# Performance work log

Hardware: AMD Instinct MI355X
Metric: run time of the kernel (lower is better)

The kernel has to match this reference:

```python
import jax, jax.numpy as jnp
import numpy as np

I_SIZE = 512
H_SIZE = 1024


def _wn(v, g):
    # weight_norm: W = g * v / ||v|| per output row (dim=0 in torch => norm over input dim)
    return v * (g / jnp.linalg.norm(v, axis=1))[:, None]


def setup_inputs() -> dict:
    key = jax.random.key(0)
    ks = jax.random.split(key, 8)
    B, S, I, H = 16, 512, I_SIZE, H_SIZE
    s_i = 1.0 / np.sqrt(I)
    s_h = 1.0 / np.sqrt(H)
    return {
        "x": jax.random.normal(ks[0], (B, S, I), jnp.float32),
        "mask": jnp.ones((B, S), jnp.float32),
        "wmx_v": jax.random.uniform(ks[1], (H, I), jnp.float32, -s_i, s_i),
        "wmx_g": jnp.ones((H,), jnp.float32),
        "wmh_v": jax.random.uniform(ks[2], (H, H), jnp.float32, -s_h, s_h),
        "wmh_g": jnp.ones((H,), jnp.float32),
        "wx_v": jax.random.uniform(ks[3], (4 * H, I), jnp.float32, -s_i, s_i),
        "wx_g": jnp.ones((4 * H,), jnp.float32),
        "wh_v": jax.random.uniform(ks[4], (4 * H, H), jnp.float32, -s_h, s_h),
        "wh_g": jnp.ones((4 * H,), jnp.float32),
        "wh_b": jax.random.uniform(ks[5], (4 * H,), jnp.float32, -s_h, s_h),
    }


def reference(x, mask, wmx_v, wmx_g, wmh_v, wmh_g, wx_v, wx_g, wh_v, wh_g, wh_b):
    B, S, _ = x.shape
    H = wmh_v.shape[0]
    Wmx = _wn(wmx_v, wmx_g)  # [H, I]
    Wmh = _wn(wmh_v, wmh_g)  # [H, H]
    Wx = _wn(wx_v, wx_g)     # [4H, I]
    Wh = _wn(wh_v, wh_g)     # [4H, H]

    # Precompute input-side projections in parallel over the whole sequence
    mx = jnp.einsum('bsi,hi->bsh', x, Wmx)   # [B, S, H]
    zx = jnp.einsum('bsi,pi->bsp', x, Wx)    # [B, S, 4H]
    mk = mask[:, :, None]                    # [B, S, 1]

    def step(carry, inp):
        h, c = carry
        mx_t, zx_t, m_t = inp
        m = mx_t * (h @ Wmh.T)
        z = zx_t + m @ Wh.T + wh_b
        i_, f_, o_, u_ = jnp.split(z, 4, axis=1)
        i_ = jax.nn.sigmoid(i_)
        f_ = jax.nn.sigmoid(f_)
        o_ = jax.nn.sigmoid(o_)
        u_ = jnp.tanh(u_)
        c_new = f_ * c + i_ * u_
        h_new = o_ * jnp.tanh(c_new)
        # masked blend: keep previous state where mask == 0
        h_new = m_t * h_new + (1.0 - m_t) * h
        c_new = m_t * c_new + (1.0 - m_t) * c
        return (h_new, c_new), h_new

    h0 = jnp.zeros((B, H), x.dtype)
    c0 = jnp.zeros((B, H), x.dtype)
    xs = (jnp.swapaxes(mx, 0, 1), jnp.swapaxes(zx, 0, 1), jnp.swapaxes(mk, 0, 1))
    (h_fin, c_fin), hs = jax.lax.scan(step, (h0, c0), xs)
    return jnp.swapaxes(hs, 0, 1), (h_fin, c_fin)
```

## Files before the change

kernel.cpp:

```cpp
#include <hip/hip_runtime.h>


typedef __attribute__((ext_vector_type(8))) short   short8;
typedef __attribute__((ext_vector_type(4))) float   float4_;

#define HSZ (16 * 512 * 1024)

__device__ __forceinline__ short f2bf(float x) {
  unsigned u = __float_as_uint(x);
  u += 0x7FFFu + ((u >> 16) & 1u);
  return (short)(u >> 16);
}
__device__ __forceinline__ float bf2f(unsigned short s) {
  return __uint_as_float(((unsigned)s) << 16);
}
__device__ __forceinline__ float sigf(float x) { return 1.f / (1.f + __expf(-x)); }
__device__ __forceinline__ float tanhfast(float x) { return 2.f / (1.f + __expf(-2.f * x)) - 1.f; }

__device__ __forceinline__ float4_ mfma16(short8 a, short8 b, float4_ c) {
  return __builtin_amdgcn_mfma_f32_16x16x32_bf16(a, b, c, 0, 0, 0);
}

__device__ __forceinline__ unsigned ld_flag(const unsigned* p) {
  return __hip_atomic_load(p, __ATOMIC_RELAXED, __HIP_MEMORY_SCOPE_AGENT);
}
__device__ __forceinline__ void st_agent(unsigned* p, unsigned v) {
  __hip_atomic_store(p, v, __ATOMIC_RELAXED, __HIP_MEMORY_SCOPE_AGENT);
}

__global__ __launch_bounds__(256) void wnorm_kernel(
    const float* __restrict__ v, const float* __restrict__ g,
    short* __restrict__ outH, short* __restrict__ outL, int cols, int permute)
{
  int r = blockIdx.x, tid = threadIdx.x;
  int src = r;
  if (permute) {
    int bid = r >> 4, jj = (r >> 2) & 3, gg = r & 3;
    src = gg * 1024 + bid * 4 + jj;
  }
  const float* row = v + (size_t)src * cols;
  float s = 0.f;
  for (int c = tid; c < cols; c += 256) { float x = row[c]; s += x * x; }
  #pragma unroll
  for (int off = 32; off; off >>= 1) s += __shfl_down(s, off);
  __shared__ float red[4];
  if ((tid & 63) == 0) red[tid >> 6] = s;
  __syncthreads();
  float tot = red[0] + red[1] + red[2] + red[3];
  float scale = g[src] / sqrtf(tot);
  for (int c = tid; c < cols; c += 256) {
    float wv = row[c] * scale;
    short hh = f2bf(wv);
    outH[(size_t)r * cols + c] = hh;
    outL[(size_t)r * cols + c] = f2bf(wv - bf2f((unsigned short)hh));
  }
}

template <int NCOLS>
__global__ __launch_bounds__(256) void gemm_xw(
    const float* __restrict__ X,
    const short* __restrict__ WH, const short* __restrict__ WL,
    float* __restrict__ Out)
{
  constexpr int BM = 128, BN = 64, BK = 32;
  __shared__ short Ah[BM][BK + 8], Al[BM][BK + 8];
  __shared__ short Bh[BN][BK + 8], Bl[BN][BK + 8];
  const int nT = NCOLS / BN;
  const int bm = blockIdx.x / nT, bn = blockIdx.x % nT;
  const int m0 = bm * BM, n0 = bn * BN;
  const int tid = threadIdx.x, lane = tid & 63, w = tid >> 6;
  const int lo = lane & 15, hi4 = lane >> 4;
  float4_ acc[2][4] = {};

  for (int kb = 0; kb < 512; kb += BK) {
    {
      int r = tid >> 1, kh = (tid & 1) << 4;
      const float* src = X + ((size_t)(m0 + r) << 9) + kb + kh;
      short8 h0, l0, h1, l1;
      #pragma unroll
      for (int u = 0; u < 8; ++u) {
        float xv = src[u];
        short hh = f2bf(xv);
        h0[u] = hh; l0[u] = f2bf(xv - bf2f((unsigned short)hh));
      }
      #pragma unroll
      for (int u = 0; u < 8; ++u) {
        float xv = src[8 + u];
        short hh = f2bf(xv);
        h1[u] = hh; l1[u] = f2bf(xv - bf2f((unsigned short)hh));
      }
      *(short8*)&Ah[r][kh] = h0;  *(short8*)&Ah[r][kh + 8] = h1;
      *(short8*)&Al[r][kh] = l0;  *(short8*)&Al[r][kh + 8] = l1;
    }
    {
      int cc = tid & 63, kq = tid >> 6;
      *(short8*)&Bh[cc][kq * 8] =
          *(const short8*)(WH + (size_t)(n0 + cc) * 512 + kb + kq * 8);
      *(short8*)&Bl[cc][kq * 8] =
          *(const short8*)(WL + (size_t)(n0 + cc) * 512 + kb + kq * 8);
    }
    __syncthreads();
    short8 bh[4], bl[4], ah[2], al[2];
    #pragma unroll
    for (int sn = 0; sn < 4; ++sn) {
      bh[sn] = *(const short8*)&Bh[sn * 16 + lo][hi4 * 8];
      bl[sn] = *(const short8*)&Bl[sn * 16 + lo][hi4 * 8];
    }
    #pragma unroll
    for (int sm = 0; sm < 2; ++sm) {
      ah[sm] = *(const short8*)&Ah[w * 32 + sm * 16 + lo][hi4 * 8];
      al[sm] = *(const short8*)&Al[w * 32 + sm * 16 + lo][hi4 * 8];
    }
    #pragma unroll
    for (int sm = 0; sm < 2; ++sm)
      #pragma unroll
      for (int sn = 0; sn < 4; ++sn)
        acc[sm][sn] = mfma16(ah[sm], bh[sn], acc[sm][sn]);
    #pragma unroll
    for (int sm = 0; sm < 2; ++sm)
      #pragma unroll
      for (int sn = 0; sn < 4; ++sn)
        acc[sm][sn] = mfma16(al[sm], bh[sn], acc[sm][sn]);
    #pragma unroll
    for (int sm = 0; sm < 2; ++sm)
      #pragma unroll
      for (int sn = 0; sn < 4; ++sn)
        acc[sm][sn] = mfma16(ah[sm], bl[sn], acc[sm][sn]);
    __syncthreads();
  }
  #pragma unroll
  for (int sm = 0; sm < 2; ++sm)
    #pragma unroll
    for (int sn = 0; sn < 4; ++sn)
      #pragma unroll
      for (int i = 0; i < 4; ++i) {
        int row = m0 + w * 32 + sm * 16 + hi4 * 4 + i;
        int col = n0 + sn * 16 + lo;
        Out[(size_t)row * NCOLS + col] = acc[sm][sn][i];
      }
}

__global__ __launch_bounds__(256, 1) void scan_kernel(
    const float* __restrict__ mx,
    const float* __restrict__ zx,
    const float* __restrict__ mask,
    const short* __restrict__ WmhH, const short* __restrict__ WmhL,
    const short* __restrict__ WhH,  const short* __restrict__ WhL,
    const float* __restrict__ bias,
    short* __restrict__ hbH, short* __restrict__ hbL,
    short* __restrict__ mbH, short* __restrict__ mbL,
    float* __restrict__ out,
    unsigned* __restrict__ flagA,
    unsigned* __restrict__ flagB)
{
  const int blk = blockIdx.x;
  const int tid = threadIdx.x;
  const int w = tid >> 6, lane = tid & 63;
  const int lo = lane & 15, hi4 = lane >> 4;

  if (blk < 16) {
    const int bid = blk * 4 + w;
    short8 wAh[32], wAl[32];
    {
      const short* wrH = WmhH + (size_t)(bid * 16 + lo) * 1024 + hi4 * 8;
      const short* wrL = WmhL + (size_t)(bid * 16 + lo) * 1024 + hi4 * 8;
      #pragma unroll
      for (int kc = 0; kc < 32; ++kc) {
        wAh[kc] = *(const short8*)(wrH + kc * 32);
        wAl[kc] = *(const short8*)(wrL + kc * 32);
      }
    }
    for (int t = 0; t < 512; ++t) {
      const int pp = t & 1, pq = pp ^ 1;
      float mxv[4];
      #pragma unroll
      for (int i = 0; i < 4; ++i)
        mxv[i] = mx[((size_t)((hi4 * 4 + i) * 512 + t)) * 1024 + bid * 16 + lo];

      if (w == 0) {
        const unsigned tgt = (unsigned)t;
        for (;;) {
          unsigned v = ld_flag(flagB + lane * 16);
          if (__all((int)(v >= tgt))) break;
          __builtin_amdgcn_s_sleep(1);
        }
      }
      __syncthreads();
      __builtin_amdgcn_fence(__ATOMIC_ACQUIRE, "agent");

      const short* hrH = hbH + pq * 16384 + lo * 1024 + hi4 * 8;
      const short* hrL = hbL + pq * 16384 + lo * 1024 + hi4 * 8;
      float4_ a0 = {0,0,0,0}, a1 = {0,0,0,0}, a2 = {0,0,0,0};
      float4_ a3 = {0,0,0,0}, a4 = {0,0,0,0}, a5 = {0,0,0,0};
      #pragma unroll
      for (int kc = 0; kc < 32; kc += 2) {
        short8 fh0 = *(const short8*)(hrH + (kc + 0) * 32);
        short8 fl0 = *(const short8*)(hrL + (kc + 0) * 32);
        short8 fh1 = *(const short8*)(hrH + (kc + 1) * 32);
        short8 fl1 = *(const short8*)(hrL + (kc + 1) * 32);
        a0 = mfma16(fh0, wAh[kc + 0], a0);
        a1 = mfma16(fl0, wAh[kc + 0], a1);
        a2 = mfma16(fh0, wAl[kc + 0], a2);
        a3 = mfma16(fh1, wAh[kc + 1], a3);
        a4 = mfma16(fl1, wAh[kc + 1], a4);
        a5 = mfma16(fh1, wAl[kc + 1], a5);
      }
      float4_ mres = ((a0 + a1) + (a2 + a3)) + (a4 + a5);
      #pragma unroll
      for (int i = 0; i < 4; ++i) {
        const int b = hi4 * 4 + i;
        float mv = mres[i] * mxv[i];
        short mh = f2bf(mv);
        short ml = f2bf(mv - bf2f((unsigned short)mh));
        unsigned hv = (unsigned short)mh, lv2 = (unsigned short)ml;
        unsigned hp = hv  | (((unsigned)__shfl_xor((int)hv, 1)) << 16);
        unsigned lp = lv2 | (((unsigned)__shfl_xor((int)lv2, 1)) << 16);
        if ((lo & 1) == 0) {
          st_agent((unsigned*)(mbH + pp * 16384 + b * 1024 + bid * 16 + lo), hp);
          st_agent((unsigned*)(mbL + pp * 16384 + b * 1024 + bid * 16 + lo), lp);
        }
      }
      asm volatile("s_waitcnt vmcnt(0)" ::: "memory");
      __syncthreads();
      if (tid == 0) st_agent(flagA + blk * 16, (unsigned)(t + 1));
    }
  } else {
    const int ebid = (blk - 16) * 4 + w;
    const int eb = lane >> 2, ejj = lane & 3;
    const int ej = ebid * 4 + ejj;
    float h_st = 0.f, c_st = 0.f;
    float biasr[4];
    #pragma unroll
    for (int g = 0; g < 4; ++g) biasr[g] = bias[g * 1024 + ebid * 4 + ejj];

    short8 wBh[32], wBl[32];
    {
      const int g = lo & 3, jj = lo >> 2;
      const short* wrH = WhH + (size_t)(g * 1024 + ebid * 4 + jj) * 1024 + hi4 * 8;
      const short* wrL = WhL + (size_t)(g * 1024 + ebid * 4 + jj) * 1024 + hi4 * 8;
      #pragma unroll
      for (int kc = 0; kc < 32; ++kc) {
        wBh[kc] = *(const short8*)(wrH + kc * 32);
        wBl[kc] = *(const short8*)(wrL + kc * 32);
      }
    }
    __shared__ float z_s[4][16][17];

    for (int t = 0; t < 512; ++t) {
      const int pp = t & 1;
      float4_ zv = *(const float4_*)(zx + (size_t)(eb * 512 + t) * 4096 + ebid * 16 + ejj * 4);
      float mk = mask[eb * 512 + t];

      if (w == 0) {
        const unsigned tgt = (unsigned)(t + 1);
        for (;;) {
          unsigned v = 0xFFFFFFFFu;
          if (lane < 16) v = ld_flag(flagA + lane * 16);
          if (__all((int)(v >= tgt))) break;
          __builtin_amdgcn_s_sleep(1);
        }
      }
      __syncthreads();
      __builtin_amdgcn_fence(__ATOMIC_ACQUIRE, "agent");

      const short* mrH = mbH + pp * 16384 + lo * 1024 + hi4 * 8;
      const short* mrL = mbL + pp * 16384 + lo * 1024 + hi4 * 8;
      float4_ b0 = {0,0,0,0}, b1 = {0,0,0,0}, b2 = {0,0,0,0};
      float4_ b3 = {0,0,0,0}, b4 = {0,0,0,0}, b5 = {0,0,0,0};
      #pragma unroll
      for (int kc = 0; kc < 32; kc += 2) {
        short8 fh0 = *(const short8*)(mrH + (kc + 0) * 32);
        short8 fl0 = *(const short8*)(mrL + (kc + 0) * 32);
        short8 fh1 = *(const short8*)(mrH + (kc + 1) * 32);
        short8 fl1 = *(const short8*)(mrL + (kc + 1) * 32);
        b0 = mfma16(fh0, wBh[kc + 0], b0);
        b1 = mfma16(fl0, wBh[kc + 0], b1);
        b2 = mfma16(fh0, wBl[kc + 0], b2);
        b3 = mfma16(fh1, wBh[kc + 1], b3);
        b4 = mfma16(fl1, wBh[kc + 1], b4);
        b5 = mfma16(fh1, wBl[kc + 1], b5);
      }
      float4_ zres = ((b0 + b1) + (b2 + b3)) + (b4 + b5);
      #pragma unroll
      for (int i = 0; i < 4; ++i) z_s[w][hi4 * 4 + i][lo] = zres[i];
      asm volatile("s_waitcnt lgkmcnt(0)" ::: "memory");

      float zg[4];
      #pragma unroll
      for (int g = 0; g < 4; ++g)
        zg[g] = z_s[w][eb][ejj * 4 + g] + zv[g] + biasr[g];
      float ig = sigf(zg[0]), fg = sigf(zg[1]), og = sigf(zg[2]);
      float ug = tanhfast(zg[3]);
      float cn = fg * c_st + ig * ug;
      float hn = og * tanhfast(cn);
      hn = mk * hn + (1.f - mk) * h_st;
      cn = mk * cn + (1.f - mk) * c_st;
      h_st = hn; c_st = cn;

      out[(size_t)(eb * 512 + t) * 1024 + ej] = hn;
      short hh = f2bf(hn);
      short hl = f2bf(hn - bf2f((unsigned short)hh));
      unsigned hv = (unsigned short)hh, lv2 = (unsigned short)hl;
      unsigned hp = hv  | (((unsigned)__shfl_xor((int)hv, 1)) << 16);
      unsigned lp = lv2 | (((unsigned)__shfl_xor((int)lv2, 1)) << 16);
      if ((ejj & 1) == 0) {
        st_agent((unsigned*)(hbH + pp * 16384 + eb * 1024 + ej), hp);
        st_agent((unsigned*)(hbL + pp * 16384 + eb * 1024 + ej), lp);
      }
      asm volatile("s_waitcnt vmcnt(0)" ::: "memory");
      __syncthreads();
      if (tid == 0) st_agent(flagB + (blk - 16) * 16, (unsigned)(t + 1));
    }
    out[HSZ + eb * 1024 + ej] = h_st;
    out[HSZ + 16384 + eb * 1024 + ej] = c_st;
  }
}

extern "C" void kernel_launch(void* const* d_in, const int* in_sizes, int n_in,
                              void* d_out, int out_size, void* d_ws, size_t ws_size,
                              hipStream_t stream)
{
  (void)in_sizes; (void)n_in; (void)out_size; (void)ws_size;
  const float* x     = (const float*)d_in[0];
  const float* mask  = (const float*)d_in[1];
  const float* wmx_v = (const float*)d_in[2];
  const float* wmx_g = (const float*)d_in[3];
  const float* wmh_v = (const float*)d_in[4];
  const float* wmh_g = (const float*)d_in[5];
  const float* wx_v  = (const float*)d_in[6];
  const float* wx_g  = (const float*)d_in[7];
  const float* wh_v  = (const float*)d_in[8];
  const float* wh_g  = (const float*)d_in[9];
  const float* wh_b  = (const float*)d_in[10];

  char* ws = (char*)d_ws;
  const size_t FLAGA_OFF = 0;
  const size_t FLAGB_OFF = 1024;
  const size_t HBH_OFF   = 8192;
  const size_t HBL_OFF   = HBH_OFF + 65536;
  const size_t MBH_OFF   = HBL_OFF + 65536;
  const size_t MBL_OFF   = MBH_OFF + 65536;
  const size_t WMHH_OFF  = (size_t)1  << 20;
  const size_t WMHL_OFF  = (size_t)3  << 20;
  const size_t WHH_OFF   = (size_t)5  << 20;
  const size_t WHL_OFF   = (size_t)13 << 20;
  const size_t WMXH_OFF  = (size_t)21 << 20;
  const size_t WMXL_OFF  = (size_t)22 << 20;
  const size_t WXH_OFF   = (size_t)23 << 20;
  const size_t WXL_OFF   = (size_t)27 << 20;
  const size_t MX_OFF    = (size_t)32 << 20;
  const size_t ZX_OFF    = (size_t)64 << 20;

  unsigned* flagA = (unsigned*)(ws + FLAGA_OFF);
  unsigned* flagB = (unsigned*)(ws + FLAGB_OFF);
  short* hbH = (short*)(ws + HBH_OFF);
  short* hbL = (short*)(ws + HBL_OFF);
  short* mbH = (short*)(ws + MBH_OFF);
  short* mbL = (short*)(ws + MBL_OFF);
  short* WmhH = (short*)(ws + WMHH_OFF);
  short* WmhL = (short*)(ws + WMHL_OFF);
  short* WhH  = (short*)(ws + WHH_OFF);
  short* WhL  = (short*)(ws + WHL_OFF);
  short* WmxH = (short*)(ws + WMXH_OFF);
  short* WmxL = (short*)(ws + WMXL_OFF);
  short* WxH  = (short*)(ws + WXH_OFF);
  short* WxL  = (short*)(ws + WXL_OFF);
  float* mx_f = (float*)(ws + MX_OFF);
  float* zx_f = (float*)(ws + ZX_OFF);
  float* out  = (float*)d_out;

  hipMemsetAsync(ws, 0, MBL_OFF + 65536, stream);

  wnorm_kernel<<<1024, 256, 0, stream>>>(wmx_v, wmx_g, WmxH, WmxL, 512, 0);
  wnorm_kernel<<<1024, 256, 0, stream>>>(wmh_v, wmh_g, WmhH, WmhL, 1024, 0);
  wnorm_kernel<<<4096, 256, 0, stream>>>(wx_v,  wx_g,  WxH,  WxL,  512, 1);
  wnorm_kernel<<<4096, 256, 0, stream>>>(wh_v,  wh_g,  WhH,  WhL,  1024, 0);

  gemm_xw<1024><<<64 * 16, 256, 0, stream>>>(x, WmxH, WmxL, mx_f);
  gemm_xw<4096><<<64 * 64, 256, 0, stream>>>(x, WxH,  WxL,  zx_f);

  scan_kernel<<<80, 256, 0, stream>>>(mx_f, zx_f, mask, WmhH, WmhL, WhH, WhL,
                                      wh_b, hbH, hbL, mbH, mbL, out, flagA, flagB);
}
```

Baseline: 16.83 ms.

## Replace acquire fences with coherent atomic loads and AGPR-resident MFMA weights

Drops the agent-scope acquire fence after each step's barrier and instead reads the exchanged h/m buffers with relaxed agent-scope atomic 64-bit loads, so the per-step cache invalidation goes away. The MFMA calls now use inline asm that takes the weight operand directly from AGPRs, with an s_nop accumulator fence, to avoid copying weights to VGPRs. The output store of h is moved after the flag publish so it leaves the critical inter-block handoff path. This relies on hand-written hazard padding and on relaxed ordering being enough, which adds some correctness risk.

```diff
diff --git a/kernel.cpp b/kernel.cpp
--- a/kernel.cpp
+++ b/kernel.cpp
@@ -20,12 +20,27 @@
 __device__ __forceinline__ float4_ mfma16(short8 a, short8 b, float4_ c) {
   return __builtin_amdgcn_mfma_f32_16x16x32_bf16(a, b, c, 0, 0, 0);
 }
+__device__ __forceinline__ void mfma_aw(float4_& acc, short8 a, const short8& b_agpr) {
+  asm("s_nop 1\n\tv_mfma_f32_16x16x32_bf16 %0, %1, %2, %0"
+      : "+v"(acc) : "v"(a), "a"(b_agpr));
+}
+#define ACC_FENCE(x0,x1,x2,x3,x4,x5)                                   \
+  asm volatile("s_nop 7\n\ts_nop 7\n\ts_nop 7"                         \
+    : "+v"(x0), "+v"(x1), "+v"(x2), "+v"(x3), "+v"(x4), "+v"(x5))
 
 __device__ __forceinline__ unsigned ld_flag(const unsigned* p) {
   return __hip_atomic_load(p, __ATOMIC_RELAXED, __HIP_MEMORY_SCOPE_AGENT);
 }
 __device__ __forceinline__ void st_agent(unsigned* p, unsigned v) {
   __hip_atomic_store(p, v, __ATOMIC_RELAXED, __HIP_MEMORY_SCOPE_AGENT);
+}
+__device__ __forceinline__ short8 ld16_coh(const short* p) {
+  const unsigned long long* q = (const unsigned long long*)p;
+  unsigned long long x0 = __hip_atomic_load(q,     __ATOMIC_RELAXED, __HIP_MEMORY_SCOPE_AGENT);
+  unsigned long long x1 = __hip_atomic_load(q + 1, __ATOMIC_RELAXED, __HIP_MEMORY_SCOPE_AGENT);
+  union { short8 s; unsigned long long u[2]; } r;
+  r.u[0] = x0; r.u[1] = x1;
+  return r.s;
 }
 
 __global__ __launch_bounds__(256) void wnorm_kernel(
@@ -186,7 +201,7 @@
         }
       }
       __syncthreads();
-      __builtin_amdgcn_fence(__ATOMIC_ACQUIRE, "agent");
+      __builtin_amdgcn_sched_barrier(0);
 
       const short* hrH = hbH + pq * 16384 + lo * 1024 + hi4 * 8;
       const short* hrL = hbL + pq * 16384 + lo * 1024 + hi4 * 8;
@@ -194,17 +209,18 @@
       float4_ a3 = {0,0,0,0}, a4 = {0,0,0,0}, a5 = {0,0,0,0};
       #pragma unroll
       for (int kc = 0; kc < 32; kc += 2) {
-        short8 fh0 = *(const short8*)(hrH + (kc + 0) * 32);
-        short8 fl0 = *(const short8*)(hrL + (kc + 0) * 32);
-        short8 fh1 = *(const short8*)(hrH + (kc + 1) * 32);
-        short8 fl1 = *(const short8*)(hrL + (kc + 1) * 32);
-        a0 = mfma16(fh0, wAh[kc + 0], a0);
-        a1 = mfma16(fl0, wAh[kc + 0], a1);
-        a2 = mfma16(fh0, wAl[kc + 0], a2);
-        a3 = mfma16(fh1, wAh[kc + 1], a3);
-        a4 = mfma16(fl1, wAh[kc + 1], a4);
-        a5 = mfma16(fh1, wAl[kc + 1], a5);
-      }
+        short8 fh0 = ld16_coh(hrH + (kc + 0) * 32);
+        short8 fl0 = ld16_coh(hrL + (kc + 0) * 32);
+        short8 fh1 = ld16_coh(hrH + (kc + 1) * 32);
+        short8 fl1 = ld16_coh(hrL + (kc + 1) * 32);
+        mfma_aw(a0, fh0, wAh[kc + 0]);
+        mfma_aw(a1, fl0, wAh[kc + 0]);
+        mfma_aw(a2, fh0, wAl[kc + 0]);
+        mfma_aw(a3, fh1, wAh[kc + 1]);
+        mfma_aw(a4, fl1, wAh[kc + 1]);
+        mfma_aw(a5, fh1, wAl[kc + 1]);
+      }
+      ACC_FENCE(a0, a1, a2, a3, a4, a5);
       float4_ mres = ((a0 + a1) + (a2 + a3)) + (a4 + a5);
       #pragma unroll
       for (int i = 0; i < 4; ++i) {
@@ -261,7 +277,7 @@
         }
       }
       __syncthreads();
-      __builtin_amdgcn_fence(__ATOMIC_ACQUIRE, "agent");
+      __builtin_amdgcn_sched_barrier(0);
 
       const short* mrH = mbH + pp * 16384 + lo * 1024 + hi4 * 8;
       const short* mrL = mbL + pp * 16384 + lo * 1024 + hi4 * 8;
@@ -269,17 +285,18 @@
       float4_ b3 = {0,0,0,0}, b4 = {0,0,0,0}, b5 = {0,0,0,0};
       #pragma unroll
       for (int kc = 0; kc < 32; kc += 2) {
-        short8 fh0 = *(const short8*)(mrH + (kc + 0) * 32);
-        short8 fl0 = *(const short8*)(mrL + (kc + 0) * 32);
-        short8 fh1 = *(const short8*)(mrH + (kc + 1) * 32);
-        short8 fl1 = *(const short8*)(mrL + (kc + 1) * 32);
-        b0 = mfma16(fh0, wBh[kc + 0], b0);
-        b1 = mfma16(fl0, wBh[kc + 0], b1);
-        b2 = mfma16(fh0, wBl[kc + 0], b2);
-        b3 = mfma16(fh1, wBh[kc + 1], b3);
-        b4 = mfma16(fl1, wBh[kc + 1], b4);
-        b5 = mfma16(fh1, wBl[kc + 1], b5);
-      }
+        short8 fh0 = ld16_coh(mrH + (kc + 0) * 32);
+        short8 fl0 = ld16_coh(mrL + (kc + 0) * 32);
+        short8 fh1 = ld16_coh(mrH + (kc + 1) * 32);
+        short8 fl1 = ld16_coh(mrL + (kc + 1) * 32);
+        mfma_aw(b0, fh0, wBh[kc + 0]);
+        mfma_aw(b1, fl0, wBh[kc + 0]);
+        mfma_aw(b2, fh0, wBl[kc + 0]);
+        mfma_aw(b3, fh1, wBh[kc + 1]);
+        mfma_aw(b4, fl1, wBh[kc + 1]);
+        mfma_aw(b5, fh1, wBl[kc + 1]);
+      }
+      ACC_FENCE(b0, b1, b2, b3, b4, b5);
       float4_ zres = ((b0 + b1) + (b2 + b3)) + (b4 + b5);
       #pragma unroll
       for (int i = 0; i < 4; ++i) z_s[w][hi4 * 4 + i][lo] = zres[i];
@@ -297,7 +314,6 @@
       cn = mk * cn + (1.f - mk) * c_st;
       h_st = hn; c_st = cn;
 
-      out[(size_t)(eb * 512 + t) * 1024 + ej] = hn;
       short hh = f2bf(hn);
       short hl = f2bf(hn - bf2f((unsigned short)hh));
       unsigned hv = (unsigned short)hh, lv2 = (unsigned short)hl;
@@ -310,6 +326,7 @@
       asm volatile("s_waitcnt vmcnt(0)" ::: "memory");
       __syncthreads();
       if (tid == 0) st_agent(flagB + (blk - 16) * 16, (unsigned)(t + 1));
+      out[(size_t)(eb * 512 + t) * 1024 + ej] = hn;
     }
     out[HSZ + eb * 1024 + ej] = h_st;
     out[HSZ + 16384 + eb * 1024 + ej] = c_st;
```

Result: faster. 16.35 ms (-2.9%).
